# Kernel tuning notes

Hardware: AMD Instinct MI355X
Metric: run time of the kernel (lower is better)

The kernel has to match this reference:

```python
import jax, jax.numpy as jnp
import numpy as np

# ---- Cl(3,0,1) algebra constants (basis blades in bitmask order, bit k = e_k) ----
# metric: e0,e1,e2 square to +1 (p=3), e3 squares to 0 (r=1, the projective/null direction)
_METRIC = [1.0, 1.0, 1.0, 0.0]

def _cayley_table():
    C = np.zeros((16, 16, 16), dtype=np.float32)
    for a in range(16):
        for b in range(16):
            # canonical reordering sign
            s, t = 0, a >> 1
            while t:
                s += bin(t & b).count('1')
                t >>= 1
            val = -1.0 if (s & 1) else 1.0
            for k in range(4):
                if (a >> k) & 1 and (b >> k) & 1:
                    val *= _METRIC[k]
            if val != 0.0:
                C[a, b, a ^ b] += val
    return C

_C = jnp.asarray(_cayley_table())                       # [16,16,16] geometric-product table
_POPC = [bin(i).count('1') for i in range(16)]
_REV = jnp.asarray([(-1.0) ** (g * (g - 1) // 2) for g in _POPC], dtype=jnp.float32)  # reverse signs
_G2 = jnp.asarray([1.0 if g == 2 else 0.0 for g in _POPC], dtype=jnp.float32)         # grade-2 mask
_CENTERS = jnp.arange(10, dtype=jnp.float32)

def _gp(a, b):
    # geometric product for small multivector batches
    return jnp.einsum('...i,...j,ijk->...k', a, b, _C)

def _mv_exp(x, n_terms=16):
    # Taylor-series exponential of a multivector (x is a small [L,16] bivector)
    term = jnp.zeros_like(x).at[..., 0].set(1.0)
    acc = term
    for n in range(1, n_terms):
        term = _gp(term, x) / n
        acc = acc + term
    return acc


def setup_inputs() -> dict:
    key = jax.random.key(0)
    k1, k2, k3, k4 = jax.random.split(key, 4)
    B, N, D, K = 32, 100000, 16, 4
    state = jax.random.normal(k1, (B, N, D), dtype=jnp.float32)
    instruction = jax.random.normal(k2, (B, D), dtype=jnp.float32)
    remap_tables = jnp.eye(10, dtype=jnp.float32)[None].repeat(K, axis=0) \
        + 0.01 * jax.random.normal(k3, (K, 10, 10), dtype=jnp.float32)
    selector_w = jax.random.normal(k4, (K, 2), dtype=jnp.float32) / jnp.sqrt(2.0)
    selector_b = jnp.zeros((K,), dtype=jnp.float32)
    return {"state": state, "instruction": instruction, "remap_tables": remap_tables,
            "selector_w": selector_w, "selector_b": selector_b}


def reference(state, instruction, remap_tables, selector_w, selector_b):
    # ---- PGA motor sandwich product ----
    bv = instruction * _G2                                   # grade-2 projection [L,16]
    M = _mv_exp(-0.5 * bv)                                   # motor [L,16]
    M_rev = M * _REV                                         # reverse(M)
    # Precompute per-row left/right multiplication matrices (avoid [L,N,16,16] outer products)
    Lmat = jnp.einsum('li,ijk->ljk', M, _C)                  # left-mult by M:   x_j -> (M x)_k
    Rmat = jnp.einsum('lj,ijk->lik', M_rev, _C)              # right-mult by ~M: y_i -> (y ~M)_k
    tmp = jnp.einsum('lnj,ljk->lnk', state, Lmat)            # M * state
    spatial = jnp.einsum('lni,lik->lnk', tmp, Rmat)          # (M * state) * ~M   [L,N,16]

    # ---- ColorUnit: soft color remap of grade-0, occupancy into grade-4 ----
    sel_input = jnp.stack([instruction[:, 0], instruction[:, 15]], axis=-1)      # [L,2]
    table_weights = jax.nn.softmax(sel_input @ selector_w.T + selector_b, axis=-1)  # [L,K]
    blended = jnp.einsum('lk,kij->lij', table_weights, remap_tables)             # [L,10,10]
    raw_color = spatial[:, :, 0] * 9.0                                           # [L,N]
    diffs = raw_color[..., None] - _CENTERS                                      # [L,N,10]
    soft_color = jax.nn.softmax(-4.0 * diffs * diffs, axis=-1)                   # [L,N,10]
    remapped = jnp.einsum('lni,lij->lnj', soft_color, blended)                   # [L,N,10]
    new_color = jnp.einsum('lni,i->ln', remapped, _CENTERS) / 9.0
    new_occupancy = 1.0 - remapped[:, :, 0]
    out = spatial.at[:, :, 0].set(new_color).at[:, :, 15].set(new_occupancy)
    return out
```

## Files before the change

### kernel.cpp

```cpp
#include <hip/hip_runtime.h>
#include <math.h>

constexpr int cpopc(int x){ int c=0; while(x){ c += x&1; x >>= 1; } return c; }

constexpr float csign(int a, int b){
    if (a & b & 8) return 0.0f;
    int s = 0;
    for (int t = a >> 1; t; t >>= 1) s += cpopc(t & b);
    return (s & 1) ? -1.0f : 1.0f;
}

__device__ constexpr int EVEN[8] = {0,3,5,6,9,10,12,15};
__device__ constexpr int EIDX[16] = {0,-1,-1,1,-1,2,3,-1,-1,4,5,-1,6,-1,-1,7};
__device__ constexpr float REVE[8] = {1.f,-1.f,-1.f,-1.f,-1.f,-1.f,-1.f,1.f};

#define WS_STRIDE 112

__global__ void setup_kernel(const float* __restrict__ instr,
                             const float* __restrict__ remap,
                             const float* __restrict__ selw,
                             const float* __restrict__ selb,
                             float* __restrict__ ws,
                             int B, int K) {
    const int l = blockIdx.x * blockDim.x + threadIdx.x;
    if (l >= B) return;
    const float* ins = instr + l * 16;

    float bv[8];
    bv[0] = 0.f; bv[7] = 0.f;
    #pragma unroll
    for (int m = 1; m < 7; m++) bv[m] = -0.5f * ins[EVEN[m]];

    float term[8], acc[8];
    #pragma unroll
    for (int m = 0; m < 8; m++){ term[m] = (m==0) ? 1.f : 0.f; acc[m] = term[m]; }
    #pragma unroll
    for (int n = 1; n < 16; n++){
        float nt[8];
        #pragma unroll
        for (int m = 0; m < 8; m++) nt[m] = 0.f;
        #pragma unroll
        for (int ia = 0; ia < 8; ia++){
            #pragma unroll
            for (int ib = 0; ib < 8; ib++){
                const float s = csign(EVEN[ia], EVEN[ib]);
                if (s != 0.f) nt[EIDX[EVEN[ia] ^ EVEN[ib]]] += s * term[ia] * bv[ib];
            }
        }
        const float inv = 1.0f / (float)n;
        #pragma unroll
        for (int m = 0; m < 8; m++){ term[m] = nt[m] * inv; acc[m] += term[m]; }
    }

    float P[64];
    #pragma unroll
    for (int ia = 0; ia < 8; ia++)
        #pragma unroll
        for (int ib = 0; ib < 8; ib++)
            P[ia*8+ib] = acc[ia] * (acc[ib] * REVE[ib]);

    float* o = ws + (size_t)l * WS_STRIDE;
    #pragma unroll
    for (int j = 0; j < 15; j++){
        float Trow[16];
        #pragma unroll
        for (int k = 0; k < 16; k++) Trow[k] = 0.f;
        #pragma unroll
        for (int ia = 0; ia < 8; ia++){
            const int A = EVEN[ia];
            const float sa = csign(A, j);
            if (sa != 0.f){
                #pragma unroll
                for (int ib = 0; ib < 8; ib++){
                    const int Bb = EVEN[ib];
                    const float s = sa * csign(A ^ j, Bb);
                    if (s != 0.f) Trow[j ^ A ^ Bb] += s * P[ia*8+ib];
                }
            }
        }
        if (j == 0){
            o[80] = Trow[0];
        } else {
            const int g = cpopc(j);
            if (g == 1){
                const int r = (j==1)?0:((j==2)?1:((j==4)?2:3));
                o[4*r+0]=Trow[1]; o[4*r+1]=Trow[2]; o[4*r+2]=Trow[4]; o[4*r+3]=Trow[8];
            } else if (g == 2){
                const int r = (j==3)?0:((j==5)?1:((j==6)?2:((j==9)?3:((j==10)?4:5))));
                float* p = o + 16 + 8*r;
                p[0]=Trow[3]; p[1]=Trow[5];  p[2]=Trow[6];  p[3]=Trow[9];
                p[4]=Trow[10]; p[5]=Trow[12]; p[6]=0.f; p[7]=0.f;
            } else {
                const int r = (j==7)?0:((j==11)?1:((j==13)?2:3));
                float* p = o + 64 + 4*r;
                p[0]=Trow[7]; p[1]=Trow[11]; p[2]=Trow[13]; p[3]=Trow[14];
            }
        }
    }

    const float s0 = ins[0], s1 = ins[15];
    float w[8];
    float mx = -1e30f;
    for (int k = 0; k < K; k++){
        w[k] = s0 * selw[2*k] + s1 * selw[2*k+1] + selb[k];
        mx = fmaxf(mx, w[k]);
    }
    float Z = 0.f;
    for (int k = 0; k < K; k++){ w[k] = __expf(w[k] - mx); Z += w[k]; }
    const float rZ = 1.f / Z;
    for (int k = 0; k < K; k++) w[k] *= rZ;

    for (int i = 0; i < 10; i++){
        float a1 = 0.f, a2 = 0.f;
        for (int k = 0; k < K; k++){
            const float* rk = remap + (size_t)(k*10 + i) * 10;
            float rd = 0.f;
            #pragma unroll
            for (int j = 0; j < 10; j++) rd += rk[j] * (float)j;
            a1 += w[k] * rd;
            a2 += w[k] * rk[0];
        }
        o[84 + 2*i]     = a1 * (1.f / 9.f);
        o[84 + 2*i + 1] = a2;
    }
}

#define TPB 256
#define EPT 2

__device__ __forceinline__ void transform_one(
    const float* sW,
    const float4 a0, const float4 a1, const float4 a2, const float4 a3,
    float4& o0, float4& o1, float4& o2, float4& o3)
{

    const float4 g10 = *reinterpret_cast<const float4*>(sW + 0);
    const float4 g11 = *reinterpret_cast<const float4*>(sW + 4);
    const float4 g12 = *reinterpret_cast<const float4*>(sW + 8);
    const float4 g13 = *reinterpret_cast<const float4*>(sW + 12);
    const float y1 = a0.y*g10.x + a0.z*g11.x + a1.x*g12.x + a2.x*g13.x;
    const float y2 = a0.y*g10.y + a0.z*g11.y + a1.x*g12.y + a2.x*g13.y;
    const float y4 = a0.y*g10.z + a0.z*g11.z + a1.x*g12.z + a2.x*g13.z;
    const float y8 = a0.y*g10.w + a0.z*g11.w + a1.x*g12.w + a2.x*g13.w;

    float y3, y5, y6, y9, y10, y12;
    {
        const float4 ra = *reinterpret_cast<const float4*>(sW + 16);
        const float2 rb = *reinterpret_cast<const float2*>(sW + 20);
        y3  = a0.w*ra.x; y5  = a0.w*ra.y; y6  = a0.w*ra.z; y9 = a0.w*ra.w;
        y10 = a0.w*rb.x; y12 = a0.w*rb.y;
    }
    {
        const float4 ra = *reinterpret_cast<const float4*>(sW + 24);
        const float2 rb = *reinterpret_cast<const float2*>(sW + 28);
        y3  += a1.y*ra.x; y5  += a1.y*ra.y; y6  += a1.y*ra.z; y9 += a1.y*ra.w;
        y10 += a1.y*rb.x; y12 += a1.y*rb.y;
    }
    {
        const float4 ra = *reinterpret_cast<const float4*>(sW + 32);
        const float2 rb = *reinterpret_cast<const float2*>(sW + 36);
        y3  += a1.z*ra.x; y5  += a1.z*ra.y; y6  += a1.z*ra.z; y9 += a1.z*ra.w;
        y10 += a1.z*rb.x; y12 += a1.z*rb.y;
    }
    {
        const float4 ra = *reinterpret_cast<const float4*>(sW + 40);
        const float2 rb = *reinterpret_cast<const float2*>(sW + 44);
        y3  += a2.y*ra.x; y5  += a2.y*ra.y; y6  += a2.y*ra.z; y9 += a2.y*ra.w;
        y10 += a2.y*rb.x; y12 += a2.y*rb.y;
    }
    {
        const float4 ra = *reinterpret_cast<const float4*>(sW + 48);
        const float2 rb = *reinterpret_cast<const float2*>(sW + 52);
        y3  += a2.z*ra.x; y5  += a2.z*ra.y; y6  += a2.z*ra.z; y9 += a2.z*ra.w;
        y10 += a2.z*rb.x; y12 += a2.z*rb.y;
    }
    {
        const float4 ra = *reinterpret_cast<const float4*>(sW + 56);
        const float2 rb = *reinterpret_cast<const float2*>(sW + 60);
        y3  += a3.x*ra.x; y5  += a3.x*ra.y; y6  += a3.x*ra.z; y9 += a3.x*ra.w;
        y10 += a3.x*rb.x; y12 += a3.x*rb.y;
    }

    const float4 g30 = *reinterpret_cast<const float4*>(sW + 64);
    const float4 g31 = *reinterpret_cast<const float4*>(sW + 68);
    const float4 g32 = *reinterpret_cast<const float4*>(sW + 72);
    const float4 g33 = *reinterpret_cast<const float4*>(sW + 76);
    const float y7  = a1.w*g30.x + a2.w*g31.x + a3.y*g32.x + a3.z*g33.x;
    const float y11 = a1.w*g30.y + a2.w*g31.y + a3.y*g32.y + a3.z*g33.y;
    const float y13 = a1.w*g30.z + a2.w*g31.z + a3.y*g32.z + a3.z*g33.z;
    const float y14 = a1.w*g30.w + a2.w*g31.w + a3.y*g32.w + a3.z*g33.w;

    const float raw  = (sW[80] * a0.x) * 9.f;
    const float ncf  = fminf(fmaxf(rintf(raw), 0.f), 9.f);
    const float dmin = raw - ncf;
    const float mlog = -4.f * dmin * dmin;
    float Z = 0.f, c1 = 0.f, c2 = 0.f;
    #pragma unroll
    for (int i = 0; i < 10; i++){
        const float d  = raw - (float)i;
        const float ev = __expf(-4.f*d*d - mlog);
        const float2 v = reinterpret_cast<const float2*>(sW + 84)[i];
        Z += ev; c1 += ev * v.x; c2 += ev * v.y;
    }
    const float rZ = 1.f / Z;

    o0 = make_float4(c1 * rZ, y1,  y2,  y3);
    o1 = make_float4(y4,      y5,  y6,  y7);
    o2 = make_float4(y8,      y9,  y10, y11);
    o3 = make_float4(y12,     y13, y14, 1.f - c2 * rZ);
}

__global__ __launch_bounds__(TPB, 4) void apply_kernel(
    const float* __restrict__ state, const float* __restrict__ ws,
    float* __restrict__ out, int N)
{
    const int l = blockIdx.y;
    __shared__ float sW[WS_STRIDE];
    if (threadIdx.x < WS_STRIDE/4)
        reinterpret_cast<float4*>(sW)[threadIdx.x] =
            reinterpret_cast<const float4*>(ws + (size_t)l * WS_STRIDE)[threadIdx.x];
    __syncthreads();

    const int tid    = blockIdx.x * TPB + threadIdx.x;
    const int stride = gridDim.x * TPB;
    const float4* __restrict__ sp = reinterpret_cast<const float4*>(state) + (size_t)l * N * 4;
    float4*       __restrict__ op = reinterpret_cast<float4*>(out)        + (size_t)l * N * 4;

    const int n0 = tid;
    const int n1 = tid + stride;
    const bool v0 = n0 < N;
    const bool v1 = n1 < N;

    float4 a0,a1,a2,a3, b0,b1,b2,b3;
    if (v0){
        const float4* p = sp + (size_t)n0 * 4;
        a0 = p[0]; a1 = p[1]; a2 = p[2]; a3 = p[3];
    } else {
        a0 = a1 = a2 = a3 = make_float4(0.f,0.f,0.f,0.f);
    }
    if (v1){
        const float4* p = sp + (size_t)n1 * 4;
        b0 = p[0]; b1 = p[1]; b2 = p[2]; b3 = p[3];
    } else {
        b0 = b1 = b2 = b3 = make_float4(0.f,0.f,0.f,0.f);
    }

    float4 o0,o1,o2,o3, q0,q1,q2,q3;
    transform_one(sW, a0,a1,a2,a3, o0,o1,o2,o3);
    transform_one(sW, b0,b1,b2,b3, q0,q1,q2,q3);

    if (v0){
        float4* p = op + (size_t)n0 * 4;
        p[0] = o0; p[1] = o1; p[2] = o2; p[3] = o3;
    }
    if (v1){
        float4* p = op + (size_t)n1 * 4;
        p[0] = q0; p[1] = q1; p[2] = q2; p[3] = q3;
    }
}

extern "C" void kernel_launch(void* const* d_in, const int* in_sizes, int n_in,
                              void* d_out, int out_size, void* d_ws, size_t ws_size,
                              hipStream_t stream) {
    const float* state = (const float*)d_in[0];
    const float* instr = (const float*)d_in[1];
    const float* remap = (const float*)d_in[2];
    const float* selw  = (const float*)d_in[3];
    const float* selb  = (const float*)d_in[4];
    float* ws  = (float*)d_ws;
    float* out = (float*)d_out;

    const int B = in_sizes[1] / 16;
    const int N = in_sizes[0] / (16 * B);
    const int K = in_sizes[4];

    setup_kernel<<<dim3((B + 63) / 64), 64, 0, stream>>>(instr, remap, selw, selb, ws, B, K);

    const int groups = (N + TPB * EPT - 1) / (TPB * EPT);
    apply_kernel<<<dim3(groups, B), TPB, 0, stream>>>(state, ws, out, N);
}
```

Measured before the change: 489.4 us.

## Stage state through swizzled shared memory for coalesced global loads and stores

Replaces per-thread strided float4x4 loads and stores with a cooperative copy in which consecutive threads touch consecutive float4s. The tile goes through shared memory with an XOR-like swizzle to avoid bank conflicts, then each thread reads its element's four float4s from LDS. Each block now processes chunks of 256 elements twice. This adds LDS traffic and barriers, and there is a possible WAR hazard on sIn/sOut across loop iterations because no barrier follows the store phase.

```diff
diff --git a/kernel.cpp b/kernel.cpp
--- a/kernel.cpp
+++ b/kernel.cpp
@@ -126,7 +126,10 @@
 }
 
 #define TPB 256
-#define EPT 2
+#define CHUNK 256
+#define CPB 2
+
+__device__ __forceinline__ int swz(int e, int c){ return 4*e + ((c + (e>>1)) & 3); }
 
 __device__ __forceinline__ void transform_one(
     const float* sW,
@@ -215,47 +218,56 @@
     float* __restrict__ out, int N)
 {
     const int l = blockIdx.y;
-    __shared__ float sW[WS_STRIDE];
-    if (threadIdx.x < WS_STRIDE/4)
-        reinterpret_cast<float4*>(sW)[threadIdx.x] =
-            reinterpret_cast<const float4*>(ws + (size_t)l * WS_STRIDE)[threadIdx.x];
-    __syncthreads();
-
-    const int tid    = blockIdx.x * TPB + threadIdx.x;
-    const int stride = gridDim.x * TPB;
+    const int t = threadIdx.x;
+
+    __shared__ float  sW[WS_STRIDE];
+    __shared__ float4 sIn [CHUNK*4];
+    __shared__ float4 sOut[CHUNK*4];
+
+    if (t < WS_STRIDE/4)
+        reinterpret_cast<float4*>(sW)[t] =
+            reinterpret_cast<const float4*>(ws + (size_t)l * WS_STRIDE)[t];
+
     const float4* __restrict__ sp = reinterpret_cast<const float4*>(state) + (size_t)l * N * 4;
-    float4*       __restrict__ op = reinterpret_cast<float4*>(out)        + (size_t)l * N * 4;
-
-    const int n0 = tid;
-    const int n1 = tid + stride;
-    const bool v0 = n0 < N;
-    const bool v1 = n1 < N;
-
-    float4 a0,a1,a2,a3, b0,b1,b2,b3;
-    if (v0){
-        const float4* p = sp + (size_t)n0 * 4;
-        a0 = p[0]; a1 = p[1]; a2 = p[2]; a3 = p[3];
-    } else {
-        a0 = a1 = a2 = a3 = make_float4(0.f,0.f,0.f,0.f);
-    }
-    if (v1){
-        const float4* p = sp + (size_t)n1 * 4;
-        b0 = p[0]; b1 = p[1]; b2 = p[2]; b3 = p[3];
-    } else {
-        b0 = b1 = b2 = b3 = make_float4(0.f,0.f,0.f,0.f);
-    }
-
-    float4 o0,o1,o2,o3, q0,q1,q2,q3;
-    transform_one(sW, a0,a1,a2,a3, o0,o1,o2,o3);
-    transform_one(sW, b0,b1,b2,b3, q0,q1,q2,q3);
-
-    if (v0){
-        float4* p = op + (size_t)n0 * 4;
-        p[0] = o0; p[1] = o1; p[2] = o2; p[3] = o3;
-    }
-    if (v1){
-        float4* p = op + (size_t)n1 * 4;
-        p[0] = q0; p[1] = q1; p[2] = q2; p[3] = q3;
+    float4*       __restrict__ op = reinterpret_cast<float4*>(out)         + (size_t)l * N * 4;
+
+    const int chunk0 = blockIdx.x * CPB;
+
+    for (int cc = 0; cc < CPB; cc++){
+        const int gbase = (chunk0 + cc) * CHUNK;
+        const float4* gp = sp + (size_t)gbase * 4;
+        float4*       gq = op + (size_t)gbase * 4;
+
+        #pragma unroll
+        for (int k = 0; k < 4; k++){
+            const int n = k*TPB + t;
+            const int e = n >> 2, c = n & 3;
+            float4 v = make_float4(0.f,0.f,0.f,0.f);
+            if (gbase + e < N) v = gp[n];
+            sIn[swz(e, c)] = v;
+        }
+        __syncthreads();
+
+        {
+            const float4 a0 = sIn[swz(t,0)];
+            const float4 a1 = sIn[swz(t,1)];
+            const float4 a2 = sIn[swz(t,2)];
+            const float4 a3 = sIn[swz(t,3)];
+            float4 o0,o1,o2,o3;
+            transform_one(sW, a0,a1,a2,a3, o0,o1,o2,o3);
+            sOut[swz(t,0)] = o0;
+            sOut[swz(t,1)] = o1;
+            sOut[swz(t,2)] = o2;
+            sOut[swz(t,3)] = o3;
+        }
+        __syncthreads();
+
+        #pragma unroll
+        for (int k = 0; k < 4; k++){
+            const int n = k*TPB + t;
+            const int e = n >> 2, c = n & 3;
+            if (gbase + e < N) gq[n] = sOut[swz(e, c)];
+        }
     }
 }
 
@@ -276,6 +288,7 @@
 
     setup_kernel<<<dim3((B + 63) / 64), 64, 0, stream>>>(instr, remap, selw, selb, ws, B, K);
 
-    const int groups = (N + TPB * EPT - 1) / (TPB * EPT);
+    const int total_chunks = (N + CHUNK - 1) / CHUNK;
+    const int groups = (total_chunks + CPB - 1) / CPB;
     apply_kernel<<<dim3(groups, B), TPB, 0, stream>>>(state, ws, out, N);
 }
```

New measurement: 452.0 us. 7.6% less time.
